# Kernel optimization log

Hardware: AMD Instinct MI355X
Metric: run time of the kernel (lower is better)

The kernel has to match this reference:

```python
import jax, jax.numpy as jnp
import numpy as np

D_MODEL = 1024
N_HEADS = 16
D_HEAD = D_MODEL // N_HEADS
D_FF = 4096
EPS = 1e-5


def layer_norm(x, g, b):
    mu = jnp.mean(x, axis=-1, keepdims=True)
    var = jnp.mean(jnp.square(x - mu), axis=-1, keepdims=True)
    return (x - mu) * jax.lax.rsqrt(var + EPS) * g + b


def setup_inputs() -> dict:
    key = jax.random.key(0)
    ks = jax.random.split(key, 8)
    s = 1.0 / np.sqrt(D_MODEL)
    return {
        "x": jax.random.normal(ks[0], (2, 2048, D_MODEL), dtype=jnp.float32),
        "Wq": jax.random.normal(ks[1], (N_HEADS, D_MODEL, D_HEAD), dtype=jnp.float32) * s,
        "Wk": jax.random.normal(ks[2], (N_HEADS, D_MODEL, D_HEAD), dtype=jnp.float32) * s,
        "Wv": jax.random.normal(ks[3], (N_HEADS, D_MODEL, D_HEAD), dtype=jnp.float32) * s,
        "Wo": jax.random.normal(ks[4], (D_MODEL, D_MODEL), dtype=jnp.float32) * s,
        "bo": jnp.zeros((D_MODEL,), dtype=jnp.float32),
        "ln1_g": jnp.ones((D_MODEL,), dtype=jnp.float32),
        "ln1_b": jnp.zeros((D_MODEL,), dtype=jnp.float32),
        "ln2_g": jnp.ones((D_MODEL,), dtype=jnp.float32),
        "ln2_b": jnp.zeros((D_MODEL,), dtype=jnp.float32),
        "W1": jax.random.normal(ks[5], (D_MODEL, D_FF), dtype=jnp.float32) * s,
        "b1": jnp.zeros((D_FF,), dtype=jnp.float32),
        "W2": jax.random.normal(ks[6], (D_FF, D_MODEL), dtype=jnp.float32) * (1.0 / np.sqrt(D_FF)),
        "b2": jnp.zeros((D_MODEL,), dtype=jnp.float32),
    }


def reference(x, Wq, Wk, Wv, Wo, bo, ln1_g, ln1_b, ln2_g, ln2_b, W1, b1, W2, b2):
    # Pre-norm MHA (per-head projections batched over head axis h)
    xn = layer_norm(x, ln1_g, ln1_b)
    q = jnp.einsum("bsd,hde->bhse", xn, Wq)
    k = jnp.einsum("bsd,hde->bhse", xn, Wk)
    v = jnp.einsum("bsd,hde->bhse", xn, Wv)
    scores = jnp.einsum("bhqe,bhke->bhqk", q, k) / jnp.sqrt(jnp.float32(D_HEAD))
    w = jax.nn.softmax(scores, axis=-1)
    attn = jnp.einsum("bhqk,bhke->bhqe", w, v)  # [b,h,s,dh]
    b, h, s, dh = attn.shape
    concat = attn.transpose(0, 2, 1, 3).reshape(b, s, h * dh)  # head concat order matches torch cat
    attn_out = concat @ Wo + bo
    hidden = x + attn_out
    hn = layer_norm(hidden, ln2_g, ln2_b)
    ff = jax.nn.gelu(hn @ W1 + b1, approximate=False) @ W2 + b2  # torch nn.GELU default = exact
    return hidden + ff
```

## Files before the change

### kernel.cpp

```cpp
#include <hip/hip_runtime.h>
#include <hip/hip_bf16.h>

typedef __bf16 bf16;
typedef __bf16 bf16x4 __attribute__((ext_vector_type(4)));
typedef __bf16 bf16x8 __attribute__((ext_vector_type(8)));
typedef float  f32x4  __attribute__((ext_vector_type(4)));

static __device__ __forceinline__ f32x4 mfma16(bf16x8 a, bf16x8 b, f32x4 c) {
  return __builtin_amdgcn_mfma_f32_16x16x32_bf16(a, b, c, 0, 0, 0);
}

static __device__ __forceinline__ float fexp2(float x) {
  return __builtin_amdgcn_exp2f(x);
}

static __device__ __forceinline__ void gl_lds16(const bf16* g, bf16* l) {
  __builtin_amdgcn_global_load_lds(
      (const __attribute__((address_space(1))) void*)g,
      (__attribute__((address_space(3))) void*)l, 16, 0, 0);
}

struct TrTab {
  const float* src[6];
  bf16* dst[6];
  int R[6], C[6], ntx[6], nty[6];
  int base[7];
};

__global__ __launch_bounds__(256) void tr6_kernel(TrTab tab) {
  int bid = blockIdx.x;
  int j = 0;
  while (j < 5 && bid >= tab.base[j + 1]) ++j;
  const int local = bid - tab.base[j];
  const int R = tab.R[j], C = tab.C[j];
  const int ntx = tab.ntx[j];
  const int per_z = ntx * tab.nty[j];
  const int z = local / per_z;
  const int rem = local - z * per_z;
  const int by = rem / ntx, bx = rem - by * ntx;
  const float* in = tab.src[j];
  bf16* out = tab.dst[j];

  __shared__ bf16 tile[32][33];
  const size_t zoff = (size_t)z * R * C;
  const int tx = threadIdx.x & 31, ty = threadIdx.x >> 5;
  const int x = bx * 32 + tx;
  const int y0 = by * 32;
#pragma unroll
  for (int jj = 0; jj < 4; ++jj)
    tile[ty + jj * 8][tx] = (bf16)in[zoff + (size_t)(y0 + ty + jj * 8) * C + x];
  __syncthreads();
  const int x2 = y0 + tx;
  const int y2 = bx * 32;
#pragma unroll
  for (int jj = 0; jj < 4; ++jj)
    out[zoff + (size_t)(y2 + ty + jj * 8) * R + x2] = tile[tx][ty + jj * 8];
}

__global__ __launch_bounds__(256) void trb_kernel(const bf16* __restrict__ inp,
                                                  bf16* __restrict__ out,
                                                  int R, int C) {
  __shared__ bf16 tile[32][33];
  const size_t zoff = (size_t)blockIdx.z * R * C;
  const int tx = threadIdx.x & 31, ty = threadIdx.x >> 5;
  const int x = blockIdx.x * 32 + tx;
  const int y0 = blockIdx.y * 32;
#pragma unroll
  for (int j = 0; j < 4; ++j)
    tile[ty + j * 8][tx] = inp[zoff + (size_t)(y0 + ty + j * 8) * C + x];
  __syncthreads();
  const int x2 = y0 + tx;
  const int y2 = blockIdx.x * 32;
#pragma unroll
  for (int j = 0; j < 4; ++j)
    out[zoff + (size_t)(y2 + ty + j * 8) * R + x2] = tile[tx][ty + j * 8];
}

__global__ __launch_bounds__(256) void ln_kernel(const float* __restrict__ inp,
                                                 const float* __restrict__ g,
                                                 const float* __restrict__ bt,
                                                 bf16* __restrict__ outp) {
  const int row = blockIdx.x;
  const int t = threadIdx.x;
  f32x4 v = ((const f32x4*)inp)[row * 256 + t];
  float s = v[0] + v[1] + v[2] + v[3];
  float sq = v[0] * v[0] + v[1] * v[1] + v[2] * v[2] + v[3] * v[3];
#pragma unroll
  for (int off = 32; off > 0; off >>= 1) {
    s += __shfl_xor(s, off);
    sq += __shfl_xor(sq, off);
  }
  __shared__ float red[8];
  const int wave = t >> 6, lane = t & 63;
  if (lane == 0) {
    red[wave] = s;
    red[wave + 4] = sq;
  }
  __syncthreads();
  s = red[0] + red[1] + red[2] + red[3];
  sq = red[4] + red[5] + red[6] + red[7];
  const float mu = s * (1.0f / 1024.0f);
  const float var = sq * (1.0f / 1024.0f) - mu * mu;
  const float rstd = rsqrtf(fmaxf(var, 0.0f) + 1e-5f);
  f32x4 gg = ((const f32x4*)g)[t];
  f32x4 bb = ((const f32x4*)bt)[t];
  bf16 o[4];
#pragma unroll
  for (int i = 0; i < 4; ++i)
    o[i] = (bf16)((v[i] - mu) * rstd * gg[i] + bb[i]);
  *(uint2*)&outp[(size_t)row * 1024 + 4 * t] = *(uint2*)o;
}

enum { EPI_QKV = 0, EPI_O = 1, EPI_FF1 = 2, EPI_FF2 = 3 };

#define VMW(N) asm volatile("s_waitcnt vmcnt(" #N ")" ::: "memory")
#define BARR                        \
  do {                              \
    __builtin_amdgcn_s_barrier();   \
    asm volatile("" ::: "memory");  \
  } while (0)

template <int EPI>
__global__ __launch_bounds__(512) void gemm256(
    const bf16* __restrict__ A, const bf16* __restrict__ Bt, const int K,
    const float* __restrict__ bias, bf16* __restrict__ outB) {
  __shared__ __align__(16) bf16 sA[2][256 * 64];
  __shared__ __align__(16) bf16 sB[2][256 * 64];
  const int t = threadIdx.x;
  const int lane = t & 63, wave = t >> 6;
  const int quad = lane >> 4, l15 = lane & 15;
  const int wm = wave >> 2, wn = wave & 3;

  const int gx = gridDim.x;
  const int lin = blockIdx.y * gx + blockIdx.x;
  const int xcd = lin & 7, idx = lin >> 3;
  const int NBX = gx >> 1;
  const int m0 = ((xcd & 3) * 4 + (idx & 3)) * 256;
  const int n0 = ((xcd >> 2) * NBX + (idx >> 2)) * 256;

  const int srow = lane >> 3;
  const int scol = ((lane & 7) ^ srow) * 8;
  const int bch = (wave & 3) + (wave >> 2) * 8;

  const bf16* aS0 = A + (size_t)(m0 + wave * 8 + srow) * K + scol;
  const bf16* aS1 = aS0 + (size_t)64 * K;
  const bf16* bS0 = Bt + (size_t)(n0 + bch * 8 + srow) * K + scol;
  const bf16* bS1 = bS0 + (size_t)32 * K;
  const size_t rsk = (size_t)128 * K;

  auto stA0 = [&](int buf, int ko) {
    gl_lds16(aS0 + ko, &sA[buf][wave * 512]);
    gl_lds16(aS0 + ko + rsk, &sA[buf][(wave + 16) * 512]);
  };
  auto stB0 = [&](int buf, int ko) {
    gl_lds16(bS0 + ko, &sB[buf][bch * 512]);
    gl_lds16(bS0 + ko + rsk, &sB[buf][(bch + 16) * 512]);
  };
  auto stB1 = [&](int buf, int ko) {
    gl_lds16(bS1 + ko, &sB[buf][(bch + 4) * 512]);
    gl_lds16(bS1 + ko + rsk, &sB[buf][(bch + 20) * 512]);
  };
  auto stA1 = [&](int buf, int ko) {
    gl_lds16(aS1 + ko, &sA[buf][(wave + 8) * 512]);
    gl_lds16(aS1 + ko + rsk, &sA[buf][(wave + 24) * 512]);
  };

  f32x4 acc[8][4];
#pragma unroll
  for (int i = 0; i < 8; ++i)
#pragma unroll
    for (int j = 0; j < 4; ++j) acc[i][j] = {0.f, 0.f, 0.f, 0.f};

  bf16x8 af[4][2], bf0[2][2], bf1[2][2];

  auto ldA = [&](int buf, int mh) {
#pragma unroll
    for (int i = 0; i < 4; ++i) {
      const int row = wm * 128 + mh * 64 + i * 16 + l15;
#pragma unroll
      for (int ks = 0; ks < 2; ++ks) {
        const int col = ((ks * 4 + quad) ^ (row & 7)) * 8;
        af[i][ks] = *(const bf16x8*)&sA[buf][row * 64 + col];
      }
    }
  };
  auto ldB = [&](int buf, int nh, bf16x8 (&bfm)[2][2]) {
#pragma unroll
    for (int j = 0; j < 2; ++j) {
      const int row = wn * 64 + nh * 32 + j * 16 + l15;
#pragma unroll
      for (int ks = 0; ks < 2; ++ks) {
        const int col = ((ks * 4 + quad) ^ (row & 7)) * 8;
        bfm[j][ks] = *(const bf16x8*)&sB[buf][row * 64 + col];
      }
    }
  };
  auto mm = [&](int mh, int nh, bf16x8 (&bfm)[2][2]) {
    asm volatile("s_waitcnt lgkmcnt(0)" ::: "memory");
    __builtin_amdgcn_sched_barrier(0);
    __builtin_amdgcn_s_setprio(1);
#pragma unroll
    for (int ks = 0; ks < 2; ++ks)
#pragma unroll
      for (int i = 0; i < 4; ++i)
#pragma unroll
        for (int j = 0; j < 2; ++j)
          acc[mh * 4 + i][nh * 2 + j] =
              mfma16(af[i][ks], bfm[j][ks], acc[mh * 4 + i][nh * 2 + j]);
    __builtin_amdgcn_s_setprio(0);
    __builtin_amdgcn_sched_barrier(0);
  };

  stA0(0, 0);
  stB0(0, 0);
  stB1(0, 0);
  stA1(0, 0);
  stA0(1, 64);
  stB0(1, 64);
  stB1(1, 64);
  VMW(6);
  BARR;

  const int NT = K >> 6;
#pragma unroll 1
  for (int it = 0; it < NT; ++it) {
    const int cur = it & 1, nxt = cur ^ 1;
    const int k1 = (it + 1) * 64, k2 = (it + 2) * 64;
    ldA(cur, 0);
    ldB(cur, 0, bf0);
    if (it + 1 < NT) stA1(nxt, k1);
    BARR;
    mm(0, 0, bf0);
    BARR;
    ldB(cur, 1, bf1);
    if (it + 2 < NT) stA0(cur, k2);
    BARR;
    mm(0, 1, bf1);
    BARR;
    ldA(cur, 1);
    if (it + 2 < NT) stB0(cur, k2);
    BARR;
    mm(1, 1, bf1);
    BARR;
    if (it + 2 < NT) {
      stB1(cur, k2);
      VMW(6);
    } else if (it + 1 < NT) {
      VMW(0);
    }
    BARR;
    mm(1, 0, bf0);
    BARR;
  }

  float bv4[4] = {0.f, 0.f, 0.f, 0.f};
  if constexpr (EPI == EPI_FF1) {
#pragma unroll
    for (int ni = 0; ni < 4; ++ni) bv4[ni] = bias[n0 + wn * 64 + ni * 16 + l15];
  }
#pragma unroll
  for (int mi = 0; mi < 8; ++mi) {
#pragma unroll
    for (int r = 0; r < 4; ++r) {
      const int m = m0 + wm * 128 + mi * 16 + quad * 4 + r;
#pragma unroll
      for (int ni = 0; ni < 4; ++ni) {
        const int n = n0 + wn * 64 + ni * 16 + l15;
        float v = acc[mi][ni][r];
        if constexpr (EPI == EPI_QKV) {
          const int which = n >> 10, nn = n & 1023;
          const int h = nn >> 6, e = nn & 63;
          const int b = m >> 11, s2 = m & 2047;
          outB[(size_t)which * 4194304 +
               ((size_t)(b * 16 + h) * 2048 + s2) * 64 + e] = (bf16)v;
        } else {
          v += bv4[ni];
          v = 0.5f * v * (1.0f + erff(v * 0.70710678118654752f));
          outB[(size_t)m * 4096 + n] = (bf16)v;
        }
      }
    }
  }
}

template <int EPI, bool NARROW>
__global__ __launch_bounds__(256) void gemm_bt(
    const bf16* __restrict__ A, const bf16* __restrict__ Bt, const int K,
    const float* __restrict__ bias, const float* __restrict__ res,
    bf16* __restrict__ outB, float* __restrict__ outF) {
  constexpr int BN = NARROW ? 64 : 128;
  constexpr int NI = NARROW ? 2 : 4;
  constexpr int BCH = BN / 32;
  __shared__ __align__(16) bf16 sA[2][128 * 64];
  __shared__ __align__(16) bf16 sB[2][BN * 64];
  const int t = threadIdx.x;
  const int lane = t & 63, wave = t >> 6;
  const int quad = lane >> 4, l15 = lane & 15;
  const int wr = wave >> 1, wc = wave & 1;
  const int m0 = blockIdx.y * 128, n0 = blockIdx.x * BN;
  const int srow = lane >> 3;
  const int scol = ((lane & 7) ^ srow) * 8;

  const bf16* aPtr[4];
#pragma unroll
  for (int c = 0; c < 4; ++c)
    aPtr[c] = A + (size_t)(m0 + wave * 32 + c * 8 + srow) * K + scol;
  const bf16* bPtr[BCH];
#pragma unroll
  for (int c = 0; c < BCH; ++c)
    bPtr[c] = Bt + (size_t)(n0 + wave * (BCH * 8) + c * 8 + srow) * K + scol;

  f32x4 acc[4][NI];
#pragma unroll
  for (int i = 0; i < 4; ++i)
#pragma unroll
    for (int j = 0; j < NI; ++j) acc[i][j] = {0.f, 0.f, 0.f, 0.f};

  const int niter = K >> 6;
#pragma unroll
  for (int c = 0; c < 4; ++c)
    gl_lds16(aPtr[c], &sA[0][(wave * 4 + c) * 512]);
#pragma unroll
  for (int c = 0; c < BCH; ++c)
    gl_lds16(bPtr[c], &sB[0][(wave * BCH + c) * 512]);

  for (int it = 0; it < niter; ++it) {
    const int cur = it & 1, nxt = cur ^ 1;
    __syncthreads();
    if (it + 1 < niter) {
      const int off = (it + 1) * 64;
#pragma unroll
      for (int c = 0; c < 4; ++c)
        gl_lds16(aPtr[c] + off, &sA[nxt][(wave * 4 + c) * 512]);
#pragma unroll
      for (int c = 0; c < BCH; ++c)
        gl_lds16(bPtr[c] + off, &sB[nxt][(wave * BCH + c) * 512]);
    }
#pragma unroll
    for (int ks = 0; ks < 2; ++ks) {
      bf16x8 af[4], bfr[NI];
#pragma unroll
      for (int mi = 0; mi < 4; ++mi) {
        const int row = wr * 64 + mi * 16 + l15;
        const int col = ((ks * 4 + quad) ^ (row & 7)) * 8;
        af[mi] = *(const bf16x8*)&sA[cur][row * 64 + col];
      }
#pragma unroll
      for (int ni = 0; ni < NI; ++ni) {
        const int row = wc * (BN / 2) + ni * 16 + l15;
        const int col = ((ks * 4 + quad) ^ (row & 7)) * 8;
        bfr[ni] = *(const bf16x8*)&sB[cur][row * 64 + col];
      }
#pragma unroll
      for (int mi = 0; mi < 4; ++mi)
#pragma unroll
        for (int ni = 0; ni < NI; ++ni)
          acc[mi][ni] = mfma16(af[mi], bfr[ni], acc[mi][ni]);
    }
  }

#pragma unroll
  for (int mi = 0; mi < 4; ++mi) {
#pragma unroll
    for (int ni = 0; ni < NI; ++ni) {
      const int n = n0 + wc * (BN / 2) + ni * 16 + l15;
#pragma unroll
      for (int r = 0; r < 4; ++r) {
        const int m = m0 + wr * 64 + mi * 16 + quad * 4 + r;
        float v = acc[mi][ni][r];
        if constexpr (EPI == EPI_QKV) {
          const int which = n >> 10, nn = n & 1023;
          const int h = nn >> 6, e = nn & 63;
          const int b = m >> 11, s2 = m & 2047;
          outB[(size_t)which * 4194304 +
               ((size_t)(b * 16 + h) * 2048 + s2) * 64 + e] = (bf16)v;
        } else if constexpr (EPI == EPI_O) {
          v += bias[n] + res[(size_t)m * 1024 + n];
          outF[(size_t)m * 1024 + n] = v;
        } else if constexpr (EPI == EPI_FF1) {
          v += bias[n];
          v = 0.5f * v * (1.0f + erff(v * 0.70710678118654752f));
          outB[(size_t)m * 4096 + n] = (bf16)v;
        } else {
          v += bias[n] + res[(size_t)m * 1024 + n];
          outF[(size_t)m * 1024 + n] = v;
        }
      }
    }
  }
}

__global__ __launch_bounds__(512, 4) void attn_kernel(
    const bf16* __restrict__ q, const bf16* __restrict__ k,
    const bf16* __restrict__ vt, bf16* __restrict__ ao) {
  __shared__ __align__(16) bf16 sP[256 * 72];
  __shared__ __align__(16) bf16 sK[2][64 * 64];
  __shared__ __align__(16) bf16 sV[2][64 * 64];
  const int t = threadIdx.x;
  const int lane = t & 63, wave = t >> 6;
  const int wq = wave & 3, kh = wave >> 2;
  const int quad = lane >> 4, l15 = lane & 15;

  const int lin = blockIdx.y * 16 + blockIdx.x;
  const int sw = (lin & 7) * 64 + (lin >> 3);
  const int q0 = (sw & 15) * 128;
  const int bh = sw >> 4, b = bh >> 4, h = bh & 15;

  const bf16* Q  = q  + (size_t)bh * 2048 * 64;
  const bf16* Kp = k  + (size_t)bh * 2048 * 64 + (size_t)kh * 1024 * 64;
  const bf16* Vt = vt + (size_t)bh * 64 * 2048 + kh * 1024;
  const int srow = lane >> 3;
  const int scol = ((lane & 7) ^ srow) * 8;
  const float SCL = 0.125f * 1.4426950408889634f;

#pragma unroll
  for (int c = 0; c < 2; ++c) {
    const int chunk = wave * 2 + c;
    const int row = chunk * 8 + srow;
    gl_lds16(&Q[(size_t)(q0 + row) * 64 + scol], &sP[chunk * 512]);
  }
  __syncthreads();
  bf16x8 qf[2][2];
#pragma unroll
  for (int mi = 0; mi < 2; ++mi)
#pragma unroll
    for (int ks = 0; ks < 2; ++ks) {
      const int row = wq * 32 + mi * 16 + l15;
      const int col = ((ks * 4 + quad) ^ (row & 7)) * 8;
      qf[mi][ks] = *(const bf16x8*)&sP[row * 64 + col];
    }
  __syncthreads();

  f32x4 o[2][4];
  float ls[2] = {0.f, 0.f};
#pragma unroll
  for (int mi = 0; mi < 2; ++mi)
#pragma unroll
    for (int ne = 0; ne < 4; ++ne) o[mi][ne] = {0.f, 0.f, 0.f, 0.f};

  for (int kb = 0; kb < 16; ++kb) {
    const int kbase = kb * 64;
    __syncthreads();
#pragma unroll
    for (int c = 0; c < 2; ++c) {
      const int chunk = wq * 2 + c;
      const int row = chunk * 8 + srow;
      gl_lds16(&Kp[(size_t)(kbase + row) * 64 + scol], &sK[kh][chunk * 512]);
      gl_lds16(&Vt[(size_t)row * 2048 + kbase + scol], &sV[kh][chunk * 512]);
    }
    __syncthreads();

    f32x4 s[4][2];
#pragma unroll
    for (int ni = 0; ni < 4; ++ni)
#pragma unroll
      for (int mi = 0; mi < 2; ++mi) s[ni][mi] = {0.f, 0.f, 0.f, 0.f};
#pragma unroll
    for (int ks = 0; ks < 2; ++ks) {
      bf16x8 kf[4];
#pragma unroll
      for (int ni = 0; ni < 4; ++ni) {
        const int row = ni * 16 + l15;
        const int col = ((ks * 4 + quad) ^ (row & 7)) * 8;
        kf[ni] = *(const bf16x8*)&sK[kh][row * 64 + col];
      }
#pragma unroll
      for (int ni = 0; ni < 4; ++ni)
#pragma unroll
        for (int mi = 0; mi < 2; ++mi)
          s[ni][mi] = mfma16(kf[ni], qf[mi][ks], s[ni][mi]);
    }

#pragma unroll
    for (int mi = 0; mi < 2; ++mi)
#pragma unroll
      for (int ni = 0; ni < 4; ++ni) {
        bf16x4 p4;
#pragma unroll
        for (int r = 0; r < 4; ++r) {
          const float p = fexp2(s[ni][mi][r] * SCL);
          ls[mi] += p;
          p4[r] = (bf16)p;
        }
        *(bf16x4*)&sP[(wave * 32 + mi * 16 + l15) * 72 + ni * 16 + quad * 4] =
            p4;
      }

#pragma unroll
    for (int ksb = 0; ksb < 2; ++ksb) {
      bf16x8 vf[4];
#pragma unroll
      for (int ne = 0; ne < 4; ++ne) {
        const int row = ne * 16 + l15;
        const int col = ((ksb * 4 + quad) ^ (row & 7)) * 8;
        vf[ne] = *(const bf16x8*)&sV[kh][row * 64 + col];
      }
#pragma unroll
      for (int mi = 0; mi < 2; ++mi) {
        const bf16x8 pf = *(const bf16x8*)&sP[(wave * 32 + mi * 16 + l15) * 72 +
                                              ksb * 32 + quad * 8];
#pragma unroll
        for (int ne = 0; ne < 4; ++ne)
          o[mi][ne] = mfma16(pf, vf[ne], o[mi][ne]);
      }
    }
  }

#pragma unroll
  for (int mi = 0; mi < 2; ++mi) {
    ls[mi] += __shfl_xor(ls[mi], 16);
    ls[mi] += __shfl_xor(ls[mi], 32);
  }

  float* mo = (float*)sP;
  float* ml = (float*)sK;
  __syncthreads();
  if (kh == 1) {
    const int base = (wq * 64 + lane) * 32;
#pragma unroll
    for (int mi = 0; mi < 2; ++mi)
#pragma unroll
      for (int ne = 0; ne < 4; ++ne)
        *(f32x4*)&mo[base + (mi * 4 + ne) * 4] = o[mi][ne];
    ml[(wq * 64 + lane) * 2 + 0] = ls[0];
    ml[(wq * 64 + lane) * 2 + 1] = ls[1];
  }
  __syncthreads();
  if (kh == 0) {
    const int base = (wq * 64 + lane) * 32;
#pragma unroll
    for (int mi = 0; mi < 2; ++mi) {
#pragma unroll
      for (int ne = 0; ne < 4; ++ne) {
        const f32x4 add = *(const f32x4*)&mo[base + (mi * 4 + ne) * 4];
#pragma unroll
        for (int r = 0; r < 4; ++r) o[mi][ne][r] += add[r];
      }
      ls[mi] += ml[(wq * 64 + lane) * 2 + mi];
      ls[mi] = 1.0f / fmaxf(ls[mi], 1e-30f);
    }
#pragma unroll
    for (int mi = 0; mi < 2; ++mi) {
      float linv[4];
#pragma unroll
      for (int r = 0; r < 4; ++r) linv[r] = __shfl(ls[mi], quad * 4 + r);
#pragma unroll
      for (int ne = 0; ne < 4; ++ne)
#pragma unroll
        for (int r = 0; r < 4; ++r) {
          const int row = q0 + wq * 32 + mi * 16 + quad * 4 + r;
          const int col = h * 64 + ne * 16 + l15;
          ao[((size_t)(b * 2048 + row)) * 1024 + col] =
              (bf16)(o[mi][ne][r] * linv[r]);
        }
    }
  }
}

extern "C" void kernel_launch(void* const* d_in, const int* in_sizes, int n_in,
                              void* d_out, int out_size, void* d_ws,
                              size_t ws_size, hipStream_t stream) {
  const float* x    = (const float*)d_in[0];
  const float* Wq   = (const float*)d_in[1];
  const float* Wk   = (const float*)d_in[2];
  const float* Wv   = (const float*)d_in[3];
  const float* Wo   = (const float*)d_in[4];
  const float* bo   = (const float*)d_in[5];
  const float* ln1g = (const float*)d_in[6];
  const float* ln1b = (const float*)d_in[7];
  const float* ln2g = (const float*)d_in[8];
  const float* ln2b = (const float*)d_in[9];
  const float* W1   = (const float*)d_in[10];
  const float* b1   = (const float*)d_in[11];
  const float* W2   = (const float*)d_in[12];
  const float* b2   = (const float*)d_in[13];

  char* ws = (char*)d_ws;
  const size_t MB = 1ull << 20;
  bf16* QKVT = (bf16*)(ws);
  bf16* WqT  = QKVT;
  bf16* WkT  = (bf16*)(ws + 2 * MB);
  bf16* WvT  = (bf16*)(ws + 4 * MB);
  bf16* WoT  = (bf16*)(ws + 6 * MB);
  bf16* W1T  = (bf16*)(ws + 8 * MB);
  bf16* W2T  = (bf16*)(ws + 16 * MB);
  bf16* sh8  = (bf16*)(ws + 24 * MB);
  bf16* qb   = (bf16*)(ws + 32 * MB);
  bf16* kb   = (bf16*)(ws + 40 * MB);
  bf16* vb   = (bf16*)(ws + 48 * MB);
  bf16* vtb  = (bf16*)(ws + 56 * MB);
  bf16* h1   = (bf16*)(ws + 32 * MB);
  float* hid = (float*)(ws + 64 * MB);

  const dim3 blk(256);

  TrTab tab;
  const float* srcs[6] = {Wq, Wk, Wv, Wo, W1, W2};
  bf16* dsts[6] = {WqT, WkT, WvT, WoT, W1T, W2T};
  const int Rs[6] = {1024, 1024, 1024, 1024, 1024, 4096};
  const int Cs[6] = {64, 64, 64, 1024, 4096, 1024};
  const int Zs[6] = {16, 16, 16, 1, 1, 1};
  int base = 0;
  for (int j = 0; j < 6; ++j) {
    tab.src[j] = srcs[j];
    tab.dst[j] = dsts[j];
    tab.R[j] = Rs[j];
    tab.C[j] = Cs[j];
    tab.ntx[j] = Cs[j] / 32;
    tab.nty[j] = Rs[j] / 32;
    tab.base[j] = base;
    base += (Cs[j] / 32) * (Rs[j] / 32) * Zs[j];
  }
  tab.base[6] = base;
  tr6_kernel<<<base, blk, 0, stream>>>(tab);

  ln_kernel<<<4096, blk, 0, stream>>>(x, ln1g, ln1b, sh8);
  gemm256<EPI_QKV><<<dim3(12, 16), dim3(512), 0, stream>>>(
      sh8, QKVT, 1024, nullptr, qb);
  trb_kernel<<<dim3(2, 64, 32), blk, 0, stream>>>(vb, vtb, 2048, 64);
  attn_kernel<<<dim3(16, 32), dim3(512), 0, stream>>>(qb, kb, vtb, sh8);
  gemm_bt<EPI_O, false><<<dim3(8, 32), blk, 0, stream>>>(
      sh8, WoT, 1024, bo, x, nullptr, hid);
  ln_kernel<<<4096, blk, 0, stream>>>(hid, ln2g, ln2b, sh8);
  gemm256<EPI_FF1><<<dim3(16, 16), dim3(512), 0, stream>>>(
      sh8, W1T, 1024, b1, h1);
  gemm_bt<EPI_FF2, true><<<dim3(16, 32), blk, 0, stream>>>(
      h1, W2T, 4096, b2, hid, nullptr, (float*)d_out);

  (void)in_sizes; (void)n_in; (void)out_size; (void)ws_size;
}
```

Before: 356.0 us.

## Add dedicated triple-buffered FF2 GEMM kernel with async LDS loads

Replaces the generic gemm_bt call for the FF2 projection with a specialized kernel using 128x64 tiles, a three-stage global-to-LDS pipeline via direct global_load_lds, XOR-swizzled LDS layout, and raised wave priority around the MFMA blocks. The aim is to hide memory latency over the long K=4096 reduction and cut LDS bank conflicts. It adds another GEMM variant to maintain and uses more LDS per block, which may reduce occupancy.

```diff
diff --git a/kernel.cpp b/kernel.cpp
--- a/kernel.cpp
+++ b/kernel.cpp
@@ -390,6 +390,100 @@
   }
 }
 
+__global__ __launch_bounds__(256) void gemm_ff2(
+    const bf16* __restrict__ A, const bf16* __restrict__ Bt, const int K,
+    const float* __restrict__ bias, const float* __restrict__ res,
+    float* __restrict__ outF) {
+  constexpr int BN = 64, NI = 2, BCH = 2;
+  __shared__ __align__(16) bf16 sA[3][128 * 64];
+  __shared__ __align__(16) bf16 sB[3][BN * 64];
+  const int t = threadIdx.x;
+  const int lane = t & 63, wave = t >> 6;
+  const int quad = lane >> 4, l15 = lane & 15;
+  const int wr = wave >> 1, wc = wave & 1;
+  const int m0 = blockIdx.y * 128, n0 = blockIdx.x * BN;
+  const int srow = lane >> 3;
+  const int scol = ((lane & 7) ^ srow) * 8;
+
+  const bf16* aPtr[4];
+#pragma unroll
+  for (int c = 0; c < 4; ++c)
+    aPtr[c] = A + (size_t)(m0 + wave * 32 + c * 8 + srow) * K + scol;
+  const bf16* bPtr[BCH];
+#pragma unroll
+  for (int c = 0; c < BCH; ++c)
+    bPtr[c] = Bt + (size_t)(n0 + wave * (BCH * 8) + c * 8 + srow) * K + scol;
+
+  auto stage = [&](int buf, int off) {
+#pragma unroll
+    for (int c = 0; c < 4; ++c)
+      gl_lds16(aPtr[c] + off, &sA[buf][(wave * 4 + c) * 512]);
+#pragma unroll
+    for (int c = 0; c < BCH; ++c)
+      gl_lds16(bPtr[c] + off, &sB[buf][(wave * BCH + c) * 512]);
+  };
+
+  f32x4 acc[4][NI];
+#pragma unroll
+  for (int i = 0; i < 4; ++i)
+#pragma unroll
+    for (int j = 0; j < NI; ++j) acc[i][j] = {0.f, 0.f, 0.f, 0.f};
+
+  const int niter = K >> 6;
+  stage(0, 0);
+  stage(1, 64);
+
+#pragma unroll 1
+  for (int it = 0; it < niter; ++it) {
+    if (it + 1 < niter) {
+      VMW(6);
+    } else {
+      VMW(0);
+    }
+    BARR;
+    if (it + 2 < niter) stage((it + 2) % 3, (it + 2) * 64);
+    const int cur = it % 3;
+#pragma unroll
+    for (int ks = 0; ks < 2; ++ks) {
+      bf16x8 af[4], bfr[NI];
+#pragma unroll
+      for (int mi = 0; mi < 4; ++mi) {
+        const int row = wr * 64 + mi * 16 + l15;
+        const int col = ((ks * 4 + quad) ^ (row & 7)) * 8;
+        af[mi] = *(const bf16x8*)&sA[cur][row * 64 + col];
+      }
+#pragma unroll
+      for (int ni = 0; ni < NI; ++ni) {
+        const int row = wc * (BN / 2) + ni * 16 + l15;
+        const int col = ((ks * 4 + quad) ^ (row & 7)) * 8;
+        bfr[ni] = *(const bf16x8*)&sB[cur][row * 64 + col];
+      }
+      __builtin_amdgcn_s_setprio(1);
+#pragma unroll
+      for (int mi = 0; mi < 4; ++mi)
+#pragma unroll
+        for (int ni = 0; ni < NI; ++ni)
+          acc[mi][ni] = mfma16(af[mi], bfr[ni], acc[mi][ni]);
+      __builtin_amdgcn_s_setprio(0);
+    }
+  }
+
+#pragma unroll
+  for (int mi = 0; mi < 4; ++mi) {
+#pragma unroll
+    for (int ni = 0; ni < NI; ++ni) {
+      const int n = n0 + wc * (BN / 2) + ni * 16 + l15;
+#pragma unroll
+      for (int r = 0; r < 4; ++r) {
+        const int m = m0 + wr * 64 + mi * 16 + quad * 4 + r;
+        float v = acc[mi][ni][r];
+        v += bias[n] + res[(size_t)m * 1024 + n];
+        outF[(size_t)m * 1024 + n] = v;
+      }
+    }
+  }
+}
+
 __global__ __launch_bounds__(512, 4) void attn_kernel(
     const bf16* __restrict__ q, const bf16* __restrict__ k,
     const bf16* __restrict__ vt, bf16* __restrict__ ao) {
@@ -624,8 +718,8 @@
   ln_kernel<<<4096, blk, 0, stream>>>(hid, ln2g, ln2b, sh8);
   gemm256<EPI_FF1><<<dim3(16, 16), dim3(512), 0, stream>>>(
       sh8, W1T, 1024, b1, h1);
-  gemm_bt<EPI_FF2, true><<<dim3(16, 32), blk, 0, stream>>>(
-      h1, W2T, 4096, b2, hid, nullptr, (float*)d_out);
+  gemm_ff2<<<dim3(16, 32), blk, 0, stream>>>(
+      h1, W2T, 4096, b2, hid, (float*)d_out);
 
   (void)in_sizes; (void)n_in; (void)out_size; (void)ws_size;
 }
```

After: 356.5 us. No clear change (+0.1%).
